# Performance work log

Hardware: AMD Instinct MI355X
Metric: run time of the kernel (lower is better)

## Reference

```python
import jax, jax.numpy as jnp
import numpy as np

L = 4          # num layers
NH = 128       # hidden channels per layer
FC = 16        # frame_channel = patch^2 * C
HP = 32        # H / patch
WP = 32        # W / patch
K = 5          # filter_size
B = 8
T_PREV = 10
T_AFTER = 10
T_TOTAL = T_PREV + T_AFTER - 1  # 19 generated frames
FORGET_BIAS = 1.0


def _conv(x, w):
    # x: [B, Cin, H, W], w: [Cout, Cin, kh, kw], stride 1, SAME padding
    return jax.lax.conv_general_dilated(
        x, w, (1, 1), 'SAME', dimension_numbers=('NCHW', 'OIHW', 'NCHW'))


def _st_lstm_cell(x, h, c, m, Wx, Wh, Wm, Wo, Wl):
    # Standard PredRNN SpatioTemporalLSTMCell (bias-free convs, no layer norm)
    xc = _conv(x, Wx)   # [B, 7*NH, H, W]
    hc = _conv(h, Wh)   # [B, 4*NH, H, W]
    mc = _conv(m, Wm)   # [B, 3*NH, H, W]
    i_x, f_x, g_x, i_xp, f_xp, g_xp, o_x = jnp.split(xc, 7, axis=1)
    i_h, f_h, g_h, o_h = jnp.split(hc, 4, axis=1)
    i_m, f_m, g_m = jnp.split(mc, 3, axis=1)

    i_t = jax.nn.sigmoid(i_x + i_h)
    f_t = jax.nn.sigmoid(f_x + f_h + FORGET_BIAS)
    g_t = jnp.tanh(g_x + g_h)
    c_new = f_t * c + i_t * g_t

    i_tp = jax.nn.sigmoid(i_xp + i_m)
    f_tp = jax.nn.sigmoid(f_xp + f_m + FORGET_BIAS)
    g_tp = jnp.tanh(g_xp + g_m)
    m_new = f_tp * m + i_tp * g_tp

    mem = jnp.concatenate([c_new, m_new], axis=1)  # [B, 2*NH, H, W]
    o_t = jax.nn.sigmoid(o_x + o_h + _conv(mem, Wo))
    h_new = o_t * jnp.tanh(_conv(mem, Wl))
    return h_new, c_new, m_new


def setup_inputs() -> dict:
    key = jax.random.key(0)
    ks = jax.random.split(key, 9)
    s = jnp.float32(0.02)  # small init scale to keep gates in a sane range
    return {
        'frames_tensor': jax.random.normal(ks[0], (B, T_PREV + T_AFTER, HP, WP, FC), jnp.float32),
        'mask_true': jax.random.uniform(ks[1], (B, T_AFTER - 1, HP, WP, FC), jnp.float32),
        'Wx0': jax.random.normal(ks[2], (7 * NH, FC, K, K), jnp.float32) * s,
        'Wx': jax.random.normal(ks[3], (L - 1, 7 * NH, NH, K, K), jnp.float32) * s,
        'Wh': jax.random.normal(ks[4], (L, 4 * NH, NH, K, K), jnp.float32) * s,
        'Wm': jax.random.normal(ks[5], (L, 3 * NH, NH, K, K), jnp.float32) * s,
        'Wo': jax.random.normal(ks[6], (L, NH, 2 * NH, K, K), jnp.float32) * s,
        'Wl': jax.random.normal(ks[7], (L, NH, 2 * NH, 1, 1), jnp.float32) * s,
        'Wout': jax.random.normal(ks[8], (FC, NH, 1, 1), jnp.float32) * s,
    }


def reference(frames_tensor, mask_true, Wx0, Wx, Wh, Wm, Wo, Wl, Wout):
    # [B,T,H,W,C] -> [B,T,C,H,W]
    frames = jnp.transpose(frames_tensor, (0, 1, 4, 2, 3))
    mask = jnp.transpose(mask_true, (0, 1, 4, 2, 3))

    # For t < data_previous the input is the ground-truth frame (mask == 1);
    # afterwards it is blended with the previous generation x_gen.
    ones = jnp.ones((B, T_PREV, FC, HP, WP), frames.dtype)
    mask_seq = jnp.concatenate([ones, mask], axis=1)  # [B, T_TOTAL, C, H, W]

    frames_t = jnp.transpose(frames[:, :T_TOTAL], (1, 0, 2, 3, 4))  # [T,B,C,H,W]
    mask_t = jnp.transpose(mask_seq, (1, 0, 2, 3, 4))               # [T,B,C,H,W]

    h0 = jnp.zeros((L, B, NH, HP, WP), frames.dtype)
    c0 = jnp.zeros((L, B, NH, HP, WP), frames.dtype)
    m0 = jnp.zeros((B, NH, HP, WP), frames.dtype)
    xg0 = jnp.zeros((B, FC, HP, WP), frames.dtype)

    def step(carry, xs):
        h, c, m, x_gen = carry
        frame, msk = xs
        net = msk * frame + (1.0 - msk) * x_gen
        h_new, c_new, m = _st_lstm_cell(net, h[0], c[0], m, Wx0, Wh[0], Wm[0], Wo[0], Wl[0])
        hs, cs = [h_new], [c_new]
        for i in range(1, L):
            hi, ci, m = _st_lstm_cell(hs[-1], h[i], c[i], m, Wx[i - 1], Wh[i], Wm[i], Wo[i], Wl[i])
            hs.append(hi)
            cs.append(ci)
        x_gen = _conv(hs[-1], Wout)  # 1x1 conv, no bias
        return (jnp.stack(hs), jnp.stack(cs), m, x_gen), x_gen

    _, next_frames = jax.lax.scan(step, (h0, c0, m0, xg0), (frames_t, mask_t))
    # [T,B,C,H,W] -> [B,T,H,W,C]
    return jnp.transpose(next_frames, (1, 0, 3, 4, 2))
```

## Files before the change

### kernel.cpp

```cpp
#include <hip/hip_runtime.h>
#include <math.h>

#define TT 19
#define TPREV 10

typedef __attribute__((ext_vector_type(8))) short bf8v;
typedef __attribute__((ext_vector_type(4))) float f4v;
typedef __attribute__((ext_vector_type(16))) float f16v;

__device__ __forceinline__ float sigmoidf_(float x){ return 1.f/(1.f+expf(-x)); }
__device__ __forceinline__ unsigned short f2bf(float x){
    unsigned int u = __float_as_uint(x);
    u += 0x7FFFu + ((u>>16)&1u);
    return (unsigned short)(u>>16);
}
__device__ __forceinline__ float bf2f(unsigned short b){ return __uint_as_float(((unsigned int)b)<<16); }

#define GLDS(g, l) __builtin_amdgcn_global_load_lds( \
    (const __attribute__((address_space(1))) void*)(g),   \
    (__attribute__((address_space(3))) void*)(l), 16, 0, 0)

struct HSeg {
    const unsigned short* in;
    int cl;
    int c0;
    int nch;
    int tap0, ntaps, five;
};
struct HJob {
    const unsigned short* wt;
    float* out;
    int cout_stride, pad;
    HSeg s;
};
struct HJobs14 { HJob j[14]; };
struct HJobs9  { HJob j[9]; };

template<typename JOBS>
__global__ __launch_bounds__(256, 2) void hconvA_kernel(JOBS jobs)
{
    __shared__ unsigned short sA[16384];
    __shared__ unsigned short sH[19200];
    const int tid = threadIdx.x;

    const int nb   = gridDim.x * gridDim.y;
    const int per8 = nb >> 3;
    const int bidl = blockIdx.x + gridDim.x * blockIdx.y;
    const int g    = (bidl & 7) * per8 + (bidl >> 3);
    const int jy   = g >> 5;
    const int xt   = g & 31;
    const HJob jb = jobs.j[jy];

    const int ng0 = xt << 8;
    const int bb = ng0 >> 10, p0 = ng0 & 1023;
    const int y0 = p0 >> 5;

    const int lane = tid & 63, wv = tid >> 6;
    const int wm = (wv & 1) << 6;
    const int wn = (wv >> 1) << 7;
    const int col = lane & 31, ll5 = lane >> 5;

    int cell0[4];
#pragma unroll
    for (int ni = 0; ni < 4; ++ni) {
        const int ln = wn + ni * 32 + col;
        cell0[ni] = ((ln >> 5) + 2) * 40 + (ln & 31) + 4;
    }
    const int rowA0 = (wm + col) * 8;
    const int oA = ll5 * 1024;

    f16v acc[2][4];
#pragma unroll
    for (int i = 0; i < 2; ++i)
#pragma unroll
        for (int j = 0; j < 4; ++j) acc[i][j] = (f16v)0.f;

    const HSeg sg = jb.s;
    const unsigned short* inb = sg.in + ((size_t)bb << (10 + sg.cl));
    const unsigned short* wptr = jb.wt;
    const int ntaps = sg.ntaps;
    const int ntot = sg.nch * ntaps;

    {
        const int c0 = sg.c0;
#pragma unroll
        for (int k = 0; k < 8; ++k) {
            const int s = tid + k * 256;
            if (s < 1920) {
                const int r = s / 160;
                const int rem = s - r * 160;
                const int cc = rem >> 2, G = rem & 3;
                const int y = y0 + r - 2, x = cc - 4;
                const bool okv = ((unsigned)y < 32u) & ((unsigned)x < 32u);
                const int yc = okv ? y : 0, xc = okv ? x : 0;
                bf8v v = *(const bf8v*)(inb + ((((yc << 5) + xc)) << sg.cl) + c0 + G * 8);
                if (!okv) v = (bf8v)(short)0;
                const int cell = r * 40 + cc;
                *(bf8v*)&sH[cell * 40 + ((G ^ ((cell >> 3) & 3))) * 8] = v;
            }
        }
    }
    GLDS(wptr + tid * 8,                &sA[tid * 8]);
    GLDS(wptr + (tid + 256) * 8,        &sA[(tid + 256) * 8]);
    GLDS(wptr + 4096 + tid * 8,         &sA[4096 + tid * 8]);
    GLDS(wptr + 4096 + (tid + 256) * 8, &sA[4096 + (tid + 256) * 8]);
    wptr += 8192;

    int bcur = 0, tc = 0, ch = 0;
    for (int t = 0; t < ntot; ++t) {
        if (tc == ntaps) {
            tc = 0; ++ch;
            __syncthreads();
            const int c0 = sg.c0 + ch * 32;
#pragma unroll
            for (int k = 0; k < 8; ++k) {
                const int s = tid + k * 256;
                if (s < 1920) {
                    const int r = s / 160;
                    const int rem = s - r * 160;
                    const int cc = rem >> 2, G = rem & 3;
                    const int y = y0 + r - 2, x = cc - 4;
                    const bool okv = ((unsigned)y < 32u) & ((unsigned)x < 32u);
                    const int yc = okv ? y : 0, xc = okv ? x : 0;
                    bf8v v = *(const bf8v*)(inb + ((((yc << 5) + xc)) << sg.cl) + c0 + G * 8);
                    if (!okv) v = (bf8v)(short)0;
                    const int cell = r * 40 + cc;
                    *(bf8v*)&sH[cell * 40 + ((G ^ ((cell >> 3) & 3))) * 8] = v;
                }
            }
        }
        if (t + 2 < ntot) {
            const int b2 = (bcur + 2) & 3;
            GLDS(wptr + tid * 8,         &sA[b2 * 4096 + tid * 8]);
            GLDS(wptr + (tid + 256) * 8, &sA[b2 * 4096 + (tid + 256) * 8]);
            wptr += 4096;
        }
        int tapofs = 0;
        if (sg.five) {
            const int tap = sg.tap0 + tc;
            const int t5 = (tap * 52) >> 8;
            tapofs = (t5 - 2) * 40 + (tap - t5 * 5 - 2);
        }
        int baddr[4][2];
#pragma unroll
        for (int ni = 0; ni < 4; ++ni) {
            const int cT = cell0[ni] + tapofs;
            const int key = (cT >> 3) & 3;
            const int cb = cT * 40;
#pragma unroll
            for (int s = 0; s < 2; ++s)
                baddr[ni][s] = cb + (((s << 1) + ll5) ^ key) * 8;
        }
        if (t + 2 < ntot)      asm volatile("s_waitcnt vmcnt(4) lgkmcnt(0)" ::: "memory");
        else if (t + 1 < ntot) asm volatile("s_waitcnt vmcnt(2) lgkmcnt(0)" ::: "memory");
        else                   asm volatile("s_waitcnt vmcnt(0) lgkmcnt(0)" ::: "memory");
        __builtin_amdgcn_s_barrier();
        __builtin_amdgcn_sched_barrier(0);

        const unsigned short* sAb = &sA[bcur * 4096];
        bf8v av[2][2], bv[2][4];
#pragma unroll
        for (int s = 0; s < 2; ++s) {
#pragma unroll
            for (int mi = 0; mi < 2; ++mi)
                av[s][mi] = *(const bf8v*)&sAb[s * 2048 + oA + rowA0 + mi * 256];
#pragma unroll
            for (int ni = 0; ni < 4; ++ni)
                bv[s][ni] = *(const bf8v*)&sH[baddr[ni][s]];
        }
        __builtin_amdgcn_s_setprio(1);
#pragma unroll
        for (int s = 0; s < 2; ++s)
#pragma unroll
            for (int mi = 0; mi < 2; ++mi)
#pragma unroll
                for (int ni = 0; ni < 4; ++ni)
                    acc[mi][ni] = __builtin_amdgcn_mfma_f32_32x32x16_bf16(
                        av[s][mi], bv[s][ni], acc[mi][ni], 0, 0, 0);
        __builtin_amdgcn_s_setprio(0);
        __builtin_amdgcn_sched_barrier(0);

        bcur = (bcur + 1) & 3;
        ++tc;
    }

    const int nfix = ng0 + wn + col;
#pragma unroll
    for (int ni = 0; ni < 4; ++ni) {
        const int n = nfix + ni * 32;
        float* ob = jb.out + (size_t)n * jb.cout_stride;
#pragma unroll
        for (int mi = 0; mi < 2; ++mi) {
            const int mb = wm + mi * 32 + 4 * ll5;
            const f16v a = acc[mi][ni];
#pragma unroll
            for (int qd = 0; qd < 4; ++qd) {
                f4v v;
                v[0] = a[qd * 4 + 0]; v[1] = a[qd * 4 + 1];
                v[2] = a[qd * 4 + 2]; v[3] = a[qd * 4 + 3];
                *(f4v*)(ob + mb + qd * 8) = v;
            }
        }
    }
}

__global__ __launch_bounds__(256) void packT_kernel(
    const float* __restrict__ src, unsigned short* __restrict__ dst,
    int Cin, int srcTaps, int rowOff, int ci0, int ntaps, int tap0,
    int ciMax, int total)
{
    const int idx = blockIdx.x * 256 + threadIdx.x;
    if (idx >= total) return;
    const int j = idx & 7;
    const int row = (idx >> 3) & 127;
    const int q = (idx >> 10) & 3;
    const int at = idx >> 12;
    const int ch = at / ntaps;
    const int tap = tap0 + (at - ch * ntaps);
    const int ci = ci0 + ch * 32 + q * 8 + j;
    float v = 0.f;
    if (ci < ciMax)
        v = src[((size_t)(rowOff + row) * Cin + ci) * srcTaps + tap];
    dst[idx] = f2bf(v);
}

__global__ __launch_bounds__(256) void net_kernel(
    const float* __restrict__ frames, const float* __restrict__ mask,
    const float* __restrict__ xgen, unsigned short* __restrict__ net, int t)
{
    const int idx = blockIdx.x * 256 + threadIdx.x;
    const int n = idx >> 5, ch = idx & 31;
    float v = 0.f;
    if (ch < 16) {
        const int b = n >> 10, p = n & 1023;
        const float fr = frames[((((size_t)b * 20 + t) << 10) + p) * 16 + ch];
        if (t < TPREV) v = fr;
        else {
            const float mk = mask[((((size_t)b * 9 + (t - TPREV)) << 10) + p) * 16 + ch];
            v = mk * fr + (1.f - mk) * xgen[(size_t)n * 16 + ch];
        }
    }
    net[idx] = f2bf(v);
}

__global__ __launch_bounds__(256) void gates_kernel(
    const float* __restrict__ preA, const float* __restrict__ preB,
    float* __restrict__ c, float* __restrict__ m,
    unsigned short* __restrict__ m_bf, unsigned short* __restrict__ mem)
{
    const int idx = blockIdx.x * 256 + threadIdx.x;
    const int n = idx >> 7, ch = idx & 127;
    const float* pa = preA + (size_t)n * 896 + ch;
    const float* pb = preB + (size_t)n * 896 + ch;
    const float i_ = pa[0]   + pb[0];
    const float f_ = pa[128] + pb[128];
    const float g_ = pa[256] + pb[256];
    const float ip = pa[384] + pb[384];
    const float fp = pa[512] + pb[512];
    const float gp = pa[640] + pb[640];
    const float cn = sigmoidf_(f_ + 1.f) * c[idx] + sigmoidf_(i_) * tanhf(g_);
    const float mn = sigmoidf_(fp + 1.f) * m[idx] + sigmoidf_(ip) * tanhf(gp);
    c[idx] = cn;
    m[idx] = mn;
    m_bf[idx] = f2bf(mn);
    mem[(size_t)n * 256 + ch] = f2bf(cn);
    mem[(size_t)n * 256 + 128 + ch] = f2bf(mn);
}

__global__ __launch_bounds__(256) void hout_kernel(
    const float* __restrict__ preA, const float* __restrict__ preB,
    const float* __restrict__ opart, const float* __restrict__ lconv,
    unsigned short* __restrict__ h)
{
    const int idx = blockIdx.x * 256 + threadIdx.x;
    const int n = idx >> 7, ch = idx & 127;
    float oc = preA[(size_t)n * 896 + 768 + ch] + preB[(size_t)n * 896 + 768 + ch];
#pragma unroll
    for (int j = 0; j < 8; ++j) oc += opart[idx + (size_t)j * 1048576];
    h[idx] = f2bf(sigmoidf_(oc) * tanhf(lconv[idx]));
}

__global__ __launch_bounds__(256) void wout_kernel(
    const unsigned short* __restrict__ h3, const float* __restrict__ wo,
    float* __restrict__ xgen, float* __restrict__ out, int t)
{
    const int idx = blockIdx.x * 256 + threadIdx.x;
    const int n = idx >> 4, ch = idx & 15;
    const int b = n >> 10, p = n & 1023;
    const unsigned short* hr = h3 + (size_t)n * 128;
    const float* wr = wo + ch * 128;
    float acc = 0.f;
#pragma unroll 8
    for (int ci = 0; ci < 128; ++ci)
        acc = fmaf(bf2f(hr[ci]), wr[ci], acc);
    xgen[idx] = acc;
    out[((((size_t)b * TT + t) << 10) + p) * 16 + ch] = acc;
}

extern "C" void kernel_launch(void* const* d_in, const int* in_sizes, int n_in,
                              void* d_out, int out_size, void* d_ws, size_t ws_size,
                              hipStream_t stream)
{
    const float* frames = (const float*)d_in[0];
    const float* mask   = (const float*)d_in[1];
    const float* Wx0    = (const float*)d_in[2];
    const float* Wx     = (const float*)d_in[3];
    const float* Wh     = (const float*)d_in[4];
    const float* Wm     = (const float*)d_in[5];
    const float* Wo     = (const float*)d_in[6];
    const float* Wl     = (const float*)d_in[7];
    const float* Wout   = (const float*)d_in[8];
    float* out = (float*)d_out;

    char* base = (char*)d_ws;
    size_t off = 0;
    auto take = [&](size_t bytes) -> char* {
        char* p = base + off;
        off = (off + bytes + 255) & ~(size_t)255;
        return p;
    };
    float* c0            = (float*)take(4ull * 1048576 * 4);
    float* m32           = (float*)take((size_t)1048576 * 4);
    unsigned short* hbf  = (unsigned short*)take(4ull * 1048576 * 2);
    unsigned short* mbf  = (unsigned short*)take((size_t)1048576 * 2);
    const size_t zbytes = off;
    float* xgen          = (float*)take((size_t)131072 * 4);
    float* preA          = (float*)take((size_t)8192 * 896 * 4);
    float* preB          = (float*)take((size_t)8192 * 896 * 4);
    float* lconv         = (float*)take((size_t)1048576 * 4);
    float* opart         = (float*)take(8ull * 1048576 * 4);
    unsigned short* net  = (unsigned short*)take((size_t)262144 * 2);
    unsigned short* mem  = (unsigned short*)take((size_t)2097152 * 2);
    unsigned short* pa0xT = (unsigned short*)take(((size_t)7 * 25 * 4096 + 4096) * 2);
    unsigned short* paT0 = (unsigned short*)take(((size_t)7 * 100 * 4096 + 4096) * 2);
    unsigned short* paT1 = (unsigned short*)take(((size_t)7 * 200 * 4096 + 4096) * 2);
    unsigned short* paT2 = (unsigned short*)take(((size_t)7 * 200 * 4096 + 4096) * 2);
    unsigned short* paT3 = (unsigned short*)take(((size_t)7 * 200 * 4096 + 4096) * 2);
    unsigned short* paT[4] = { paT0, paT1, paT2, paT3 };
    unsigned short* oT   = (unsigned short*)take((4ull * 200 * 4096 + 4096) * 2);
    unsigned short* lT   = (unsigned short*)take((4ull * 8 * 4096 + 4096) * 2);

    hipMemsetAsync(d_ws, 0, zbytes, stream);

    auto packT = [&](const float* s, unsigned short* d, int Cin, int srcTaps,
                     int rowOff, int ci0, int nch, int ntaps, int tap0, int ciMax) {
        const int total = nch * ntaps * 4096;
        packT_kernel<<<(total + 255) / 256, 256, 0, stream>>>(
            s, d, Cin, srcTaps, rowOff, ci0, ntaps, tap0, ciMax, total);
    };
    const int CIMAXBIG = 1 << 30;
    for (int g = 0; g < 7; ++g) {
        packT(Wx0, pa0xT + (size_t)g * 25 * 4096, 16, 25, g * 128, 0, 1, 25, 0, 16);
        const float* hm0 = (g < 3) ? (Wh + (size_t)g * 128 * 128 * 25)
                         : (g == 6) ? (Wh + (size_t)384 * 128 * 25)
                                    : (Wm + (size_t)(g - 3) * 128 * 128 * 25);
        packT(hm0, paT0 + (size_t)g * 100 * 4096, 128, 25, 0, 0, 4, 25, 0, CIMAXBIG);
        for (int l = 1; l < 4; ++l) {
            packT(Wx + (size_t)(l - 1) * 896 * 128 * 25,
                  paT[l] + (size_t)g * 200 * 4096, 128, 25, g * 128, 0, 4, 25, 0, CIMAXBIG);
            const float* hmsrc = (g < 3) ? (Wh + ((size_t)l * 512 + g * 128) * 128 * 25)
                               : (g == 6) ? (Wh + ((size_t)l * 512 + 384) * 128 * 25)
                                          : (Wm + ((size_t)l * 384 + (g - 3) * 128) * 128 * 25);
            packT(hmsrc, paT[l] + ((size_t)g * 200 + 100) * 4096, 128, 25, 0, 0, 4, 25, 0, CIMAXBIG);
        }
    }
    for (int l = 0; l < 4; ++l) {
        packT(Wo + (size_t)l * 128 * 256 * 25, oT + (size_t)l * 200 * 4096,
              256, 25, 0, 0, 8, 25, 0, CIMAXBIG);
        packT(Wl + (size_t)l * 128 * 256, lT + (size_t)l * 8 * 4096,
              256, 1, 0, 0, 8, 1, 0, CIMAXBIG);
    }

    for (int t = 0; t < TT; ++t) {
        net_kernel<<<1024, 256, 0, stream>>>(frames, mask, xgen, net, t);
        for (int l = 0; l < 4; ++l) {
            unsigned short* hl = hbf + (size_t)l * 1048576;
            HJobs14 JA{};
            if (l == 0) {
                for (int g = 0; g < 7; ++g) {
                    const unsigned short* hmsrc = (g < 3 || g == 6) ? hl : mbf;
                    JA.j[2 * g] = HJob{ pa0xT + (size_t)g * 25 * 4096, preA + g * 128,
                                        896, 0, HSeg{ net, 5, 0, 1, 0, 25, 1 } };
                    JA.j[2 * g + 1] = HJob{ paT0 + (size_t)g * 100 * 4096, preB + g * 128,
                                            896, 0, HSeg{ hmsrc, 7, 0, 4, 0, 25, 1 } };
                }
            } else {
                for (int g = 0; g < 7; ++g) {
                    const unsigned short* hmsrc = (g < 3 || g == 6) ? hl : mbf;
                    JA.j[g] = HJob{ paT[l] + (size_t)g * 200 * 4096, preA + g * 128,
                                    896, 0, HSeg{ hbf + (size_t)(l - 1) * 1048576, 7, 0, 4, 0, 25, 1 } };
                    JA.j[7 + g] = HJob{ paT[l] + ((size_t)g * 200 + 100) * 4096, preB + g * 128,
                                        896, 0, HSeg{ hmsrc, 7, 0, 4, 0, 25, 1 } };
                }
            }
            hconvA_kernel<HJobs14><<<dim3(32, 14), 256, 0, stream>>>(JA);

            gates_kernel<<<4096, 256, 0, stream>>>(preA, preB,
                c0 + (size_t)l * 1048576, m32, mbf, mem);

            HJobs9 JB{};
            for (int jj = 0; jj < 8; ++jj)
                JB.j[jj] = HJob{ oT + ((size_t)l * 200 + jj * 25) * 4096,
                                 opart + (size_t)jj * 1048576, 128, 0,
                                 HSeg{ mem, 8, jj * 32, 1, 0, 25, 1 } };
            JB.j[8] = HJob{ lT + (size_t)l * 8 * 4096, lconv, 128, 0,
                            HSeg{ mem, 8, 0, 8, 0, 1, 0 } };
            hconvA_kernel<HJobs9><<<dim3(32, 9), 256, 0, stream>>>(JB);

            hout_kernel<<<4096, 256, 0, stream>>>(preA, preB, opart, lconv, hl);
        }
        wout_kernel<<<512, 256, 0, stream>>>(hbf + (size_t)3 * 1048576, Wout, xgen, out, t);
    }
}
```

Before: 11.82 ms.

## Use a planar LDS layout for input halos and smaller-tile kernel for output convs

Replaces the XOR-swizzled per-cell LDS layout of the input halo with a planar layout grouped by 8-channel chunk, so B-operand addresses become a fixed per-lane offset plus a per-tap offset and the per-tap address arithmetic goes away. It also drops one scheduling barrier after the MFMA block. The second conv launch per layer (the Wo/Wl jobs) now uses a new kernel with 128-pixel tiles and a double-buffered weight pipeline on a 64x9 grid, giving more blocks for that small job set. The planar layout may bring back LDS bank conflicts that the swizzle avoided, and the new kernel synchronises after every tap.

New measurement: 10.91 ms. -7.7%, faster.

```diff
diff --git a/kernel.cpp b/kernel.cpp
--- a/kernel.cpp
+++ b/kernel.cpp
@@ -36,11 +36,12 @@
 struct HJobs14 { HJob j[14]; };
 struct HJobs9  { HJob j[9]; };
 
+
 template<typename JOBS>
 __global__ __launch_bounds__(256, 2) void hconvA_kernel(JOBS jobs)
 {
     __shared__ unsigned short sA[16384];
-    __shared__ unsigned short sH[19200];
+    __shared__ unsigned short sH[15360];
     const int tid = threadIdx.x;
 
     const int nb   = gridDim.x * gridDim.y;
@@ -60,11 +61,12 @@
     const int wn = (wv >> 1) << 7;
     const int col = lane & 31, ll5 = lane >> 5;
 
-    int cell0[4];
+    int bofs0[4];
 #pragma unroll
     for (int ni = 0; ni < 4; ++ni) {
         const int ln = wn + ni * 32 + col;
-        cell0[ni] = ((ln >> 5) + 2) * 40 + (ln & 31) + 4;
+        const int cell = ((ln >> 5) + 2) * 40 + (ln & 31) + 4;
+        bofs0[ni] = cell * 8 + ll5 * 3840;
     }
     const int rowA0 = (wm + col) * 8;
     const int oA = ll5 * 1024;
@@ -95,8 +97,7 @@
                 const int yc = okv ? y : 0, xc = okv ? x : 0;
                 bf8v v = *(const bf8v*)(inb + ((((yc << 5) + xc)) << sg.cl) + c0 + G * 8);
                 if (!okv) v = (bf8v)(short)0;
-                const int cell = r * 40 + cc;
-                *(bf8v*)&sH[cell * 40 + ((G ^ ((cell >> 3) & 3))) * 8] = v;
+                *(bf8v*)&sH[(G * 480 + r * 40 + cc) * 8] = v;
             }
         }
     }
@@ -124,8 +125,7 @@
                     const int yc = okv ? y : 0, xc = okv ? x : 0;
                     bf8v v = *(const bf8v*)(inb + ((((yc << 5) + xc)) << sg.cl) + c0 + G * 8);
                     if (!okv) v = (bf8v)(short)0;
-                    const int cell = r * 40 + cc;
-                    *(bf8v*)&sH[cell * 40 + ((G ^ ((cell >> 3) & 3))) * 8] = v;
+                    *(bf8v*)&sH[(G * 480 + r * 40 + cc) * 8] = v;
                 }
             }
         }
@@ -135,21 +135,11 @@
             GLDS(wptr + (tid + 256) * 8, &sA[b2 * 4096 + (tid + 256) * 8]);
             wptr += 4096;
         }
-        int tapofs = 0;
+        int tO = 0;
         if (sg.five) {
             const int tap = sg.tap0 + tc;
             const int t5 = (tap * 52) >> 8;
-            tapofs = (t5 - 2) * 40 + (tap - t5 * 5 - 2);
-        }
-        int baddr[4][2];
-#pragma unroll
-        for (int ni = 0; ni < 4; ++ni) {
-            const int cT = cell0[ni] + tapofs;
-            const int key = (cT >> 3) & 3;
-            const int cb = cT * 40;
-#pragma unroll
-            for (int s = 0; s < 2; ++s)
-                baddr[ni][s] = cb + (((s << 1) + ll5) ^ key) * 8;
+            tO = ((t5 - 2) * 40 + (tap - t5 * 5 - 2)) * 8;
         }
         if (t + 2 < ntot)      asm volatile("s_waitcnt vmcnt(4) lgkmcnt(0)" ::: "memory");
         else if (t + 1 < ntot) asm volatile("s_waitcnt vmcnt(2) lgkmcnt(0)" ::: "memory");
@@ -166,7 +156,7 @@
                 av[s][mi] = *(const bf8v*)&sAb[s * 2048 + oA + rowA0 + mi * 256];
 #pragma unroll
             for (int ni = 0; ni < 4; ++ni)
-                bv[s][ni] = *(const bf8v*)&sH[baddr[ni][s]];
+                bv[s][ni] = *(const bf8v*)&sH[bofs0[ni] + tO + s * 7680];
         }
         __builtin_amdgcn_s_setprio(1);
 #pragma unroll
@@ -178,7 +168,6 @@
                     acc[mi][ni] = __builtin_amdgcn_mfma_f32_32x32x16_bf16(
                         av[s][mi], bv[s][ni], acc[mi][ni], 0, 0, 0);
         __builtin_amdgcn_s_setprio(0);
-        __builtin_amdgcn_sched_barrier(0);
 
         bcur = (bcur + 1) & 3;
         ++tc;
@@ -187,6 +176,117 @@
     const int nfix = ng0 + wn + col;
 #pragma unroll
     for (int ni = 0; ni < 4; ++ni) {
+        const int n = nfix + ni * 32;
+        float* ob = jb.out + (size_t)n * jb.cout_stride;
+#pragma unroll
+        for (int mi = 0; mi < 2; ++mi) {
+            const int mb = wm + mi * 32 + 4 * ll5;
+            const f16v a = acc[mi][ni];
+#pragma unroll
+            for (int qd = 0; qd < 4; ++qd) {
+                f4v v;
+                v[0] = a[qd * 4 + 0]; v[1] = a[qd * 4 + 1];
+                v[2] = a[qd * 4 + 2]; v[3] = a[qd * 4 + 3];
+                *(f4v*)(ob + mb + qd * 8) = v;
+            }
+        }
+    }
+}
+
+template<typename JOBS>
+__global__ __launch_bounds__(256) void hconv_kernel(JOBS jobs)
+{
+    __shared__ unsigned short sA[8192];
+    __shared__ unsigned short sH[10240];
+    const HJob jb = jobs.j[blockIdx.y];
+    const int tid = threadIdx.x;
+
+    const int ng0 = blockIdx.x * 128;
+    const int bb = ng0 >> 10, p0 = ng0 & 1023;
+    const int y0 = p0 >> 5;
+
+    const int lane = tid & 63, wv = tid >> 6;
+    const int wm = (wv & 1) << 6;
+    const int wn = (wv >> 1) << 6;
+    const int col = lane & 31, ll5 = lane >> 5;
+
+    int bofs0[2];
+#pragma unroll
+    for (int ni = 0; ni < 2; ++ni) {
+        const int ln = wn + ni * 32 + col;
+        const int cell = ((ln >> 5) + 2) * 40 + (ln & 31) + 4;
+        bofs0[ni] = cell * 8 + ll5 * 2560;
+    }
+
+    f16v acc[2][2];
+#pragma unroll
+    for (int i = 0; i < 2; ++i)
+#pragma unroll
+        for (int j = 0; j < 2; ++j) acc[i][j] = (f16v)0.f;
+
+    const HSeg sg = jb.s;
+    const unsigned short* inb = sg.in + ((size_t)bb << (10 + sg.cl));
+    const unsigned short* wptr = jb.wt;
+    int buf = 0;
+    bool first = true;
+    for (int ch = 0; ch < sg.nch; ++ch) {
+        const int c0 = sg.c0 + ch * 32;
+#pragma unroll
+        for (int k = 0; k < 5; ++k) {
+            const int s = tid + k * 256;
+            const int r = s / 160;
+            const int rem = s - r * 160;
+            const int cc = rem >> 2, G = rem & 3;
+            const int y = y0 + r - 2, x = cc - 4;
+            const bool okv = ((unsigned)y < 32u) & ((unsigned)x < 32u);
+            const int yc = okv ? y : 0, xc = okv ? x : 0;
+            bf8v v = *(const bf8v*)(inb + ((((yc << 5) + xc)) << sg.cl) + c0 + G * 8);
+            if (!okv) v = (bf8v)(short)0;
+            *(bf8v*)&sH[(G * 320 + r * 40 + cc) * 8] = v;
+        }
+        if (first) {
+            GLDS(wptr + tid * 8,         &sA[tid * 8]);
+            GLDS(wptr + (tid + 256) * 8, &sA[(tid + 256) * 8]);
+            wptr += 4096;
+            first = false;
+        }
+        __syncthreads();
+        for (int t = 0; t < sg.ntaps; ++t) {
+            GLDS(wptr + tid * 8,         &sA[(buf ^ 1) * 4096 + tid * 8]);
+            GLDS(wptr + (tid + 256) * 8, &sA[(buf ^ 1) * 4096 + (tid + 256) * 8]);
+            wptr += 4096;
+            int tO = 0;
+            if (sg.five) {
+                const int tap = sg.tap0 + t;
+                const int t5 = (tap * 52) >> 8;
+                tO = ((t5 - 2) * 40 + (tap - t5 * 5 - 2)) * 8;
+            }
+            const unsigned short* sAb = &sA[buf * 4096];
+#pragma unroll
+            for (int s = 0; s < 2; ++s) {
+                const int o = s * 2 + ll5;
+                bf8v av[2], bv[2];
+#pragma unroll
+                for (int mi = 0; mi < 2; ++mi)
+                    av[mi] = *(const bf8v*)&sAb[(o * 128 + wm + mi * 32 + col) * 8];
+#pragma unroll
+                for (int ni = 0; ni < 2; ++ni)
+                    bv[ni] = *(const bf8v*)&sH[bofs0[ni] + tO + s * 5120];
+#pragma unroll
+                for (int mi = 0; mi < 2; ++mi)
+#pragma unroll
+                    for (int ni = 0; ni < 2; ++ni)
+                        acc[mi][ni] = __builtin_amdgcn_mfma_f32_32x32x16_bf16(
+                            av[mi], bv[ni], acc[mi][ni], 0, 0, 0);
+            }
+            __syncthreads();
+            buf ^= 1;
+        }
+    }
+
+    const int nfix = ng0 + wn + col;
+#pragma unroll
+    for (int ni = 0; ni < 2; ++ni) {
         const int n = nfix + ni * 32;
         float* ob = jb.out + (size_t)n * jb.cout_stride;
 #pragma unroll
@@ -405,7 +505,7 @@
                                  HSeg{ mem, 8, jj * 32, 1, 0, 25, 1 } };
             JB.j[8] = HJob{ lT + (size_t)l * 8 * 4096, lconv, 128, 0,
                             HSeg{ mem, 8, 0, 8, 0, 1, 0 } };
-            hconvA_kernel<HJobs9><<<dim3(32, 9), 256, 0, stream>>>(JB);
+            hconv_kernel<HJobs9><<<dim3(64, 9), 256, 0, stream>>>(JB);
 
             hout_kernel<<<4096, 256, 0, stream>>>(preA, preB, opart, lconv, hl);
         }
```
